# Performance work log

Measured on AMD Instinct MI355X. Metric: run time of the kernel, lower is better.

The kernel has to match this reference:

```python
import jax, jax.numpy as jnp
import numpy as np

B, S, H, E, V, EXTRA = 256, 400, 512, 512, 50257, 100
EMB = H + E  # embedding_size


def setup_inputs() -> dict:
    key = jax.random.key(0)
    ks = jax.random.split(key, 20)
    sd = lambda *shape: 1.0 / np.sqrt(shape[-1])
    d = {
        "input_step": jax.random.normal(ks[0], (B, EMB), jnp.float32),
        "last_hidden": jax.random.normal(ks[1], (1, B, H), jnp.float32),
        "encoder_outputs": jax.random.normal(ks[2], (S, B, H), jnp.float32),
        "enc_batch_extend_vocab": jax.random.randint(ks[3], (S, B), 0, V + EXTRA, jnp.int32),
        "extra_zeros": jnp.zeros((B, EXTRA), jnp.float32),
        "attn_masks": jnp.ones((B, S), jnp.float32),
        "W_ih": jax.random.normal(ks[4], (3 * H, EMB), jnp.float32) * sd(EMB),
        "W_hh": jax.random.normal(ks[5], (3 * H, H), jnp.float32) * sd(H),
        "b_ih": jax.random.normal(ks[6], (3 * H,), jnp.float32) * 0.02,
        "b_hh": jax.random.normal(ks[7], (3 * H,), jnp.float32) * 0.02,
        "attn_W": jax.random.normal(ks[8], (H, 2 * H), jnp.float32) * sd(2 * H),
        "attn_b": jax.random.normal(ks[9], (H,), jnp.float32) * 0.02,
        "attn_v": jax.random.normal(ks[10], (H,), jnp.float32) * sd(H),
        "concat_W": jax.random.normal(ks[11], (H, 2 * H), jnp.float32) * sd(2 * H),
        "concat_b": jax.random.normal(ks[12], (H,), jnp.float32) * 0.02,
        "out_W": jax.random.normal(ks[13], (V, H), jnp.float32) * sd(H),
        "out_b": jax.random.normal(ks[14], (V,), jnp.float32) * 0.02,
        "pgen_W": jax.random.normal(ks[15], (1, 2 * H + EMB), jnp.float32) * sd(2 * H + EMB),
        "pgen_b": jax.random.normal(ks[16], (1,), jnp.float32) * 0.02,
        "sig_W": jax.random.normal(ks[17], (1, H), jnp.float32) * sd(H),
        "sig_b": jax.random.normal(ks[18], (1,), jnp.float32) * 0.02,
    }
    return d


def reference(input_step, last_hidden, encoder_outputs, enc_batch_extend_vocab,
              extra_zeros, attn_masks, W_ih, W_hh, b_ih, b_hh, attn_W, attn_b,
              attn_v, concat_W, concat_b, out_W, out_b, pgen_W, pgen_b,
              sig_W, sig_b):
    # eval-mode dropout is identity
    embedded = input_step                      # [B, EMB]
    h_prev = last_hidden[0]                    # [B, H] (nlayers = 1)

    # --- single GRU step (PyTorch gate layout: r, z, n) ---
    gi = embedded @ W_ih.T + b_ih              # [B, 3H]
    gh = h_prev @ W_hh.T + b_hh                # [B, 3H]
    i_r, i_z, i_n = jnp.split(gi, 3, axis=1)
    h_r, h_z, h_n = jnp.split(gh, 3, axis=1)
    r = jax.nn.sigmoid(i_r + h_r)
    z = jax.nn.sigmoid(i_z + h_z)
    n = jnp.tanh(i_n + r * h_n)
    rnn_output = (1.0 - z) * n + z * h_prev    # [B, H]
    hidden = rnn_output[None]                  # [1, B, H]

    # --- concat attention: v^T tanh(W [h; enc]) over source positions ---
    h_exp = jnp.broadcast_to(rnn_output[None], encoder_outputs.shape)   # [S, B, H]
    energy = jnp.tanh(
        jnp.concatenate([h_exp, encoder_outputs], axis=-1) @ attn_W.T + attn_b
    )                                          # [S, B, H]
    scores = jnp.einsum('sbh,h->bs', energy, attn_v)                    # [B, S]
    scores = jnp.where(attn_masks > 0, scores, jnp.float32(-1e18))
    attn_w = jax.nn.softmax(scores, axis=1)                             # [B, S]
    context = jnp.einsum('bs,sbh->bh', attn_w, encoder_outputs)         # [B, H]

    # --- pgen gate: sigmoid(gelu(Linear([hidden; context; emb]))) ---
    hidden_inp = h_prev                        # last_hidden flattened, [B, H]
    pgen_in = jnp.concatenate([hidden_inp, context, embedded], axis=1)
    pgen = jax.nn.sigmoid(jax.nn.gelu(pgen_in @ pgen_W.T + pgen_b,
                                      approximate=False))               # [B, 1]

    # --- vocab distribution + copy distribution, fused chain ---
    concat_out = jax.nn.gelu(
        jnp.concatenate([rnn_output, context], axis=1) @ concat_W.T + concat_b,
        approximate=False)                     # [B, H]
    logits = concat_out @ out_W.T + out_b      # [B, V]
    vocab_dist = jax.nn.softmax(logits, axis=1)
    vocab_dist = jnp.concatenate([vocab_dist, extra_zeros], axis=1)     # [B, V+EXTRA]
    vocab_dist = pgen * vocab_dist
    attn_dist = (1.0 - pgen) * attn_w          # [B, S]

    idx = enc_batch_extend_vocab.T             # [B, S]
    rows = jnp.arange(vocab_dist.shape[0])[:, None]
    final = vocab_dist.at[rows, idx].add(attn_dist)                     # scatter_add

    out = jax.nn.log_softmax(jnp.log(final + 1e-5), axis=1)

    attn_weights = attn_w.T                    # [S, B]
    sig_hid = rnn_output @ sig_W.T + sig_b     # [B, 1]
    return out, hidden, attn_weights, sig_hid
```

## Files before the change

### kernel.cpp

```cpp
#include <hip/hip_runtime.h>
#include <hip/hip_bf16.h>
#include <math.h>

#define BB 256
#define SS 400
#define HH 512
#define EMBD 1024
#define VV 50257
#define VE 50357
#define O_HID  12891392
#define O_ATT  13022464
#define O_SIG  13124864

typedef __attribute__((ext_vector_type(8))) short s8v;
typedef __attribute__((ext_vector_type(4))) float f4v;

__device__ __forceinline__ float sigmoidf(float x) { return 1.f / (1.f + expf(-x)); }
__device__ __forceinline__ float geluf(float x) { return 0.5f * x * (1.f + erff(x * 0.70710678118654752f)); }

__device__ __forceinline__ void split2_pack(float x0, float x1, unsigned& hp, unsigned& lp) {
  unsigned u0 = __float_as_uint(x0), u1 = __float_as_uint(x1);
  hp = (u0 >> 16) | (u1 & 0xFFFF0000u);
  float d0 = x0 - __uint_as_float(u0 & 0xFFFF0000u);
  float d1 = x1 - __uint_as_float(u1 & 0xFFFF0000u);
  lp = (__float_as_uint(d0) >> 16) | (__float_as_uint(d1) & 0xFFFF0000u);
}

template<int ACT>
__global__ __launch_bounds__(256) void gemm_nt(const float* __restrict__ A, int lda,
                                               const float* __restrict__ W, int ldw,
                                               const float* __restrict__ bias,
                                               float* __restrict__ C, int ldc,
                                               int N, int K) {
  __shared__ __align__(16) float As[16][68];
  __shared__ __align__(16) float Ws[16][68];
  const int tid = threadIdx.x;
  const int m0 = blockIdx.x * 64, n0 = blockIdx.y * 64;
  const int tx = tid & 15, ty = tid >> 4;
  const int lr = tid >> 2;
  const int lk = (tid & 3) * 4;
  float acc[4][4] = {};
  for (int k0 = 0; k0 < K; k0 += 16) {
    float4 a4, w4;
    a4 = *(const float4*)(A + (size_t)(m0 + lr) * lda + k0 + lk);
    int wrow = n0 + lr;
    if (wrow < N) w4 = *(const float4*)(W + (size_t)wrow * ldw + k0 + lk);
    else          w4 = make_float4(0.f, 0.f, 0.f, 0.f);
    __syncthreads();
    As[lk + 0][lr] = a4.x; As[lk + 1][lr] = a4.y; As[lk + 2][lr] = a4.z; As[lk + 3][lr] = a4.w;
    Ws[lk + 0][lr] = w4.x; Ws[lk + 1][lr] = w4.y; Ws[lk + 2][lr] = w4.z; Ws[lk + 3][lr] = w4.w;
    __syncthreads();
#pragma unroll
    for (int k = 0; k < 16; ++k) {
      float4 av = *(const float4*)&As[k][ty * 4];
      float4 wv = *(const float4*)&Ws[k][tx * 4];
      float am[4] = {av.x, av.y, av.z, av.w};
      float wn[4] = {wv.x, wv.y, wv.z, wv.w};
#pragma unroll
      for (int i = 0; i < 4; ++i)
#pragma unroll
        for (int j = 0; j < 4; ++j) acc[i][j] += am[i] * wn[j];
    }
  }
#pragma unroll
  for (int i = 0; i < 4; ++i) {
    int row = m0 + ty * 4 + i;
#pragma unroll
    for (int j = 0; j < 4; ++j) {
      int col = n0 + tx * 4 + j;
      if (col < N) {
        float val = acc[i][j] + bias[col];
        if (ACT == 1) val = geluf(val);
        C[(size_t)row * ldc + col] = val;
      }
    }
  }
}

__global__ __launch_bounds__(256) void gru_gemms(const float* __restrict__ input_step,
                                                 const float* __restrict__ last_hidden,
                                                 const float* __restrict__ W_ih,
                                                 const float* __restrict__ W_hh,
                                                 const float* __restrict__ b_ih,
                                                 const float* __restrict__ b_hh,
                                                 float* __restrict__ gi, float* __restrict__ gh) {
  __shared__ __align__(16) float As[16][68];
  __shared__ __align__(16) float Ws[16][68];
  const bool isGi = blockIdx.y < 24;
  const float* A = isGi ? input_step : last_hidden;
  const float* W = isGi ? W_ih : W_hh;
  const float* bias = isGi ? b_ih : b_hh;
  float* C = isGi ? gi : gh;
  const int lda = isGi ? 1024 : 512;
  const int K = isGi ? 1024 : 512;
  const int n0 = (isGi ? blockIdx.y : blockIdx.y - 24) * 64;
  const int m0 = blockIdx.x * 64;
  const int tid = threadIdx.x;
  const int tx = tid & 15, ty = tid >> 4;
  const int lr = tid >> 2;
  const int lk = (tid & 3) * 4;
  float acc[4][4] = {};
  for (int k0 = 0; k0 < K; k0 += 16) {
    float4 a4 = *(const float4*)(A + (size_t)(m0 + lr) * lda + k0 + lk);
    float4 w4 = *(const float4*)(W + (size_t)(n0 + lr) * lda + k0 + lk);
    __syncthreads();
    As[lk + 0][lr] = a4.x; As[lk + 1][lr] = a4.y; As[lk + 2][lr] = a4.z; As[lk + 3][lr] = a4.w;
    Ws[lk + 0][lr] = w4.x; Ws[lk + 1][lr] = w4.y; Ws[lk + 2][lr] = w4.z; Ws[lk + 3][lr] = w4.w;
    __syncthreads();
#pragma unroll
    for (int k = 0; k < 16; ++k) {
      float4 av = *(const float4*)&As[k][ty * 4];
      float4 wv = *(const float4*)&Ws[k][tx * 4];
      float am[4] = {av.x, av.y, av.z, av.w};
      float wn[4] = {wv.x, wv.y, wv.z, wv.w};
#pragma unroll
      for (int i = 0; i < 4; ++i)
#pragma unroll
        for (int j = 0; j < 4; ++j) acc[i][j] += am[i] * wn[j];
    }
  }
#pragma unroll
  for (int i = 0; i < 4; ++i) {
    int row = m0 + ty * 4 + i;
#pragma unroll
    for (int j = 0; j < 4; ++j) {
      int col = n0 + tx * 4 + j;
      C[(size_t)row * 1536 + col] = acc[i][j] + bias[col];
    }
  }
}

__global__ __launch_bounds__(256) void gru_combine(const float* __restrict__ gi, const float* __restrict__ gh,
                                                   const float* __restrict__ hprev,
                                                   float* __restrict__ rnn, float* __restrict__ hid_out,
                                                   float* __restrict__ cin) {
  int idx = blockIdx.x * 256 + threadIdx.x;
  int b = idx >> 9, j = idx & 511;
  const float* gib = gi + (size_t)b * 1536;
  const float* ghb = gh + (size_t)b * 1536;
  float r = sigmoidf(gib[j] + ghb[j]);
  float z = sigmoidf(gib[512 + j] + ghb[512 + j]);
  float n = tanhf(gib[1024 + j] + r * ghb[1024 + j]);
  float h = hprev[idx];
  float o = (1.f - z) * n + z * h;
  rnn[idx] = o;
  hid_out[idx] = o;
  cin[(size_t)b * 1024 + j] = o;
}

__global__ __launch_bounds__(256) void pack_split(const float* __restrict__ src, int ld, int col0, int rows,
                                                  unsigned short* __restrict__ dhi,
                                                  unsigned short* __restrict__ dlo) {
  int idx = blockIdx.x * 256 + threadIdx.x;
  int l = idx & 63;
  int kb = (idx >> 6) & 15;
  int jb = idx >> 10;
  int j = jb * 16 + (l & 15);
  int k0 = kb * 32 + (l >> 4) * 8;
  float4 x0 = make_float4(0.f, 0.f, 0.f, 0.f), x1 = x0;
  if (j < rows) {
    const float* p = src + (size_t)j * ld + col0 + k0;
    x0 = *(const float4*)p;
    x1 = *(const float4*)(p + 4);
  }
  unsigned h0, l0, h1, l1, h2, l2, h3, l3;
  split2_pack(x0.x, x0.y, h0, l0);
  split2_pack(x0.z, x0.w, h1, l1);
  split2_pack(x1.x, x1.y, h2, l2);
  split2_pack(x1.z, x1.w, h3, l3);
  *(uint4*)(dhi + (size_t)idx * 8) = make_uint4(h0, h1, h2, h3);
  *(uint4*)(dlo + (size_t)idx * 8) = make_uint4(l0, l1, l2, l3);
}

__global__ __launch_bounds__(256, 2) void attn_mfma(const float* __restrict__ enc,
                                                    const unsigned short* __restrict__ BhiP,
                                                    const unsigned short* __restrict__ BloP,
                                                    const float* __restrict__ hW,
                                                    const float* __restrict__ v,
                                                    float* __restrict__ scores) {
  __shared__ __align__(16) unsigned short AhiL[2 * 4 * 66 * 8];
  __shared__ __align__(16) unsigned short AloL[2 * 4 * 66 * 8];

  const int tid = threadIdx.x;
  const int R0 = blockIdx.x * 64;
  const int jhalf = blockIdx.y;
  const int lane = tid & 63;
  const int w = tid >> 6;
  const int jbBase = jhalf * 16 + w * 4;
  const int g = lane >> 4;
  const int l16 = lane & 15;

  const int ar = tid >> 2;
  const int akc = tid & 3;
  const float* aptr = enc + (size_t)(R0 + ar) * 512 + akc * 8;

  const unsigned short* bh0 = BhiP + lane * 8;
  const unsigned short* bl0 = BloP + lane * 8;

  f4v acc[4][4];
#pragma unroll
  for (int rt = 0; rt < 4; ++rt)
#pragma unroll
    for (int ct = 0; ct < 4; ++ct) acc[rt][ct] = (f4v){0.f, 0.f, 0.f, 0.f};

  {
    float4 x0 = *(const float4*)(aptr);
    float4 x1 = *(const float4*)(aptr + 4);
    unsigned h0, l0, h1, l1, h2, l2, h3, l3;
    split2_pack(x0.x, x0.y, h0, l0);
    split2_pack(x0.z, x0.w, h1, l1);
    split2_pack(x1.x, x1.y, h2, l2);
    split2_pack(x1.z, x1.w, h3, l3);
    int wb = akc * 66 + ar;
    *(uint4*)&AhiL[wb * 8] = make_uint4(h0, h1, h2, h3);
    *(uint4*)&AloL[wb * 8] = make_uint4(l0, l1, l2, l3);
  }
  s8v BH[4], BL[4];
#pragma unroll
  for (int ct = 0; ct < 4; ++ct) {
    const int fo = ((jbBase + ct) * 16 + 0) * 512;
    BH[ct] = *(const s8v*)(bh0 + fo);
    BL[ct] = *(const s8v*)(bl0 + fo);
  }
  __syncthreads();

  for (int t = 0; t < 16; ++t) {
    const int k0 = t * 32;
    float4 pa0, pa1;
    if (t < 15) {
      pa0 = *(const float4*)(aptr + k0 + 32);
      pa1 = *(const float4*)(aptr + k0 + 36);
    }
    const int rb = ((t & 1) * 4 + g) * 66 + l16;
#pragma unroll
    for (int rt = 0; rt < 4; ++rt) {
      s8v ah = *(const s8v*)&AhiL[(rb + rt * 16) * 8];
      s8v al = *(const s8v*)&AloL[(rb + rt * 16) * 8];
#pragma unroll
      for (int ct = 0; ct < 4; ++ct) {
        acc[rt][ct] = __builtin_amdgcn_mfma_f32_16x16x32_bf16(ah, BH[ct], acc[rt][ct], 0, 0, 0);
        acc[rt][ct] = __builtin_amdgcn_mfma_f32_16x16x32_bf16(ah, BL[ct], acc[rt][ct], 0, 0, 0);
        acc[rt][ct] = __builtin_amdgcn_mfma_f32_16x16x32_bf16(al, BH[ct], acc[rt][ct], 0, 0, 0);
      }
    }
    if (t < 15) {
#pragma unroll
      for (int ct = 0; ct < 4; ++ct) {
        const int fo = ((jbBase + ct) * 16 + (t + 1)) * 512;
        BH[ct] = *(const s8v*)(bh0 + fo);
        BL[ct] = *(const s8v*)(bl0 + fo);
      }
    }
    if (t < 15) {
      unsigned h0, l0, h1, l1, h2, l2, h3, l3;
      split2_pack(pa0.x, pa0.y, h0, l0);
      split2_pack(pa0.z, pa0.w, h1, l1);
      split2_pack(pa1.x, pa1.y, h2, l2);
      split2_pack(pa1.z, pa1.w, h3, l3);
      int wb = (((t + 1) & 1) * 4 + akc) * 66 + ar;
      *(uint4*)&AhiL[wb * 8] = make_uint4(h0, h1, h2, h3);
      *(uint4*)&AloL[wb * 8] = make_uint4(l0, l1, l2, l3);
    }
    __syncthreads();
  }

  float sp[4][4] = {};
#pragma unroll
  for (int ct = 0; ct < 4; ++ct) {
    int j = jhalf * 256 + w * 64 + ct * 16 + l16;
    float vj = v[j];
    const float* hWj = hW + j;
#pragma unroll
    for (int rt = 0; rt < 4; ++rt) {
#pragma unroll
      for (int q = 0; q < 4; ++q) {
        int rl = rt * 16 + g * 4 + q;
        int b = (R0 + rl) & 255;
        float e = acc[rt][ct][q] + hWj[(size_t)b * 512];
        sp[rt][q] += tanhf(e) * vj;
      }
    }
  }

  __syncthreads();
  float* sredf = (float*)AhiL;
#pragma unroll
  for (int rt = 0; rt < 4; ++rt)
#pragma unroll
    for (int q = 0; q < 4; ++q) {
      float s = sp[rt][q];
      s += __shfl_xor(s, 1); s += __shfl_xor(s, 2);
      s += __shfl_xor(s, 4); s += __shfl_xor(s, 8);
      if (l16 == 0) sredf[(rt * 16 + g * 4 + q) * 4 + w] = s;
    }
  __syncthreads();
  if (tid < 64) {
    float s = sredf[tid * 4 + 0] + sredf[tid * 4 + 1] + sredf[tid * 4 + 2] + sredf[tid * 4 + 3];
    int r = R0 + tid;
    int b = r & 255, si = r >> 8;
    atomicAdd(scores + b * 400 + si, s);
  }
}

__global__ __launch_bounds__(256, 2) void logits_mfma(const float* __restrict__ A,
                                                      const float* __restrict__ W,
                                                      const float* __restrict__ bias,
                                                      float* __restrict__ out) {
  __shared__ __align__(16) unsigned short AhiL[2 * 4 * 66 * 8];
  __shared__ __align__(16) unsigned short AloL[2 * 4 * 66 * 8];

  const int tid = threadIdx.x;
  const int R0 = blockIdx.x * 64;
  const int C0 = blockIdx.y * 256;
  const int lane = tid & 63;
  const int w = tid >> 6;
  const int g = lane >> 4;
  const int l16 = lane & 15;

  const int ar = tid >> 2;
  const int akc = tid & 3;
  const float* aptr = A + (size_t)(R0 + ar) * 512 + akc * 8;

  int jc[4]; bool jok[4];
#pragma unroll
  for (int ct = 0; ct < 4; ++ct) {
    jc[ct] = C0 + w * 64 + ct * 16 + l16;
    jok[ct] = jc[ct] < VV;
  }

  f4v acc[4][4];
#pragma unroll
  for (int rt = 0; rt < 4; ++rt)
#pragma unroll
    for (int ct = 0; ct < 4; ++ct) acc[rt][ct] = (f4v){0.f, 0.f, 0.f, 0.f};

  {
    float4 pa0 = *(const float4*)(aptr);
    float4 pa1 = *(const float4*)(aptr + 4);
    unsigned h0, l0, h1, l1, h2, l2, h3, l3;
    split2_pack(pa0.x, pa0.y, h0, l0);
    split2_pack(pa0.z, pa0.w, h1, l1);
    split2_pack(pa1.x, pa1.y, h2, l2);
    split2_pack(pa1.z, pa1.w, h3, l3);
    int wb = akc * 66 + ar;
    *(uint4*)&AhiL[wb * 8] = make_uint4(h0, h1, h2, h3);
    *(uint4*)&AloL[wb * 8] = make_uint4(l0, l1, l2, l3);
  }
  __syncthreads();

#pragma unroll 2
  for (int t = 0; t < 16; ++t) {
    const int k0 = t * 32;
    s8v BH[4], BL[4];
#pragma unroll
    for (int ct = 0; ct < 4; ++ct) {
      const float* wp = W + (size_t)(jok[ct] ? jc[ct] : 0) * 512 + k0 + g * 8;
      float4 b0 = *(const float4*)wp;
      float4 b1 = *(const float4*)(wp + 4);
      if (!jok[ct]) { b0 = make_float4(0.f, 0.f, 0.f, 0.f); b1 = b0; }
      unsigned h0, l0, h1, l1, h2, l2, h3, l3;
      split2_pack(b0.x, b0.y, h0, l0);
      split2_pack(b0.z, b0.w, h1, l1);
      split2_pack(b1.x, b1.y, h2, l2);
      split2_pack(b1.z, b1.w, h3, l3);
      uint4 ph = make_uint4(h0, h1, h2, h3);
      uint4 pl = make_uint4(l0, l1, l2, l3);
      BH[ct] = *(s8v*)&ph; BL[ct] = *(s8v*)&pl;
    }
    float4 pa0, pa1;
    if (t < 15) {
      pa0 = *(const float4*)(aptr + k0 + 32);
      pa1 = *(const float4*)(aptr + k0 + 36);
    }
    const int rb = ((t & 1) * 4 + g) * 66 + l16;
#pragma unroll
    for (int rt = 0; rt < 4; ++rt) {
      s8v ah = *(const s8v*)&AhiL[(rb + rt * 16) * 8];
      s8v al = *(const s8v*)&AloL[(rb + rt * 16) * 8];
#pragma unroll
      for (int ct = 0; ct < 4; ++ct) {
        acc[rt][ct] = __builtin_amdgcn_mfma_f32_16x16x32_bf16(ah, BH[ct], acc[rt][ct], 0, 0, 0);
        acc[rt][ct] = __builtin_amdgcn_mfma_f32_16x16x32_bf16(ah, BL[ct], acc[rt][ct], 0, 0, 0);
        acc[rt][ct] = __builtin_amdgcn_mfma_f32_16x16x32_bf16(al, BH[ct], acc[rt][ct], 0, 0, 0);
      }
    }
    if (t < 15) {
      unsigned h0, l0, h1, l1, h2, l2, h3, l3;
      split2_pack(pa0.x, pa0.y, h0, l0);
      split2_pack(pa0.z, pa0.w, h1, l1);
      split2_pack(pa1.x, pa1.y, h2, l2);
      split2_pack(pa1.z, pa1.w, h3, l3);
      int wb = (((t + 1) & 1) * 4 + akc) * 66 + ar;
      *(uint4*)&AhiL[wb * 8] = make_uint4(h0, h1, h2, h3);
      *(uint4*)&AloL[wb * 8] = make_uint4(l0, l1, l2, l3);
    }
    __syncthreads();
  }

#pragma unroll
  for (int ct = 0; ct < 4; ++ct) {
    if (!jok[ct]) continue;
    float bj = bias[jc[ct]];
#pragma unroll
    for (int rt = 0; rt < 4; ++rt) {
      int row = R0 + rt * 16 + g * 4;
#pragma unroll
      for (int q = 0; q < 4; ++q)
        out[(size_t)(row + q) * VE + jc[ct]] = acc[rt][ct][q] + bj;
    }
  }
}

__global__ __launch_bounds__(256) void softmax_k(const float* __restrict__ scores,
                                                 const float* __restrict__ masks,
                                                 float* __restrict__ attnw, float* __restrict__ attnT) {
  int b = blockIdx.x, tid = threadIdx.x;
  __shared__ float red[4];
  float m = -3e38f;
  for (int s = tid; s < 400; s += 256) {
    float sc = (masks[b * 400 + s] > 0.f) ? scores[b * 400 + s] : -1e18f;
    m = fmaxf(m, sc);
  }
#pragma unroll
  for (int o = 32; o; o >>= 1) m = fmaxf(m, __shfl_xor(m, o));
  if ((tid & 63) == 0) red[tid >> 6] = m;
  __syncthreads();
  m = fmaxf(fmaxf(red[0], red[1]), fmaxf(red[2], red[3]));
  __syncthreads();
  float z = 0.f;
  for (int s = tid; s < 400; s += 256) {
    float sc = (masks[b * 400 + s] > 0.f) ? scores[b * 400 + s] : -1e18f;
    z += expf(sc - m);
  }
#pragma unroll
  for (int o = 32; o; o >>= 1) z += __shfl_xor(z, o);
  if ((tid & 63) == 0) red[tid >> 6] = z;
  __syncthreads();
  z = red[0] + red[1] + red[2] + red[3];
  float inv = 1.f / z;
  for (int s = tid; s < 400; s += 256) {
    float sc = (masks[b * 400 + s] > 0.f) ? scores[b * 400 + s] : -1e18f;
    float w = expf(sc - m) * inv;
    attnw[b * 400 + s] = w;
    attnT[s * 256 + b] = w;
  }
}

__global__ __launch_bounds__(1024) void context_k(const float* __restrict__ enc,
                                                  const float* __restrict__ attnw,
                                                  float* __restrict__ ctx, float* __restrict__ cin) {
  int b = blockIdx.x, tid = threadIdx.x;
  __shared__ float w[400];
  __shared__ float part[4][512];
  for (int s = tid; s < 400; s += 1024) w[s] = attnw[b * 400 + s];
  __syncthreads();
  const int h = (tid & 255) * 2;
  const int sq = tid >> 8;
  const float* p = enc + (size_t)b * 512 + h;
  float cx = 0.f, cy = 0.f;
  const int s0 = sq * 100;
#pragma unroll 4
  for (int s = s0; s < s0 + 100; ++s) {
    float2 e = *(const float2*)(p + (size_t)s * 131072);
    cx += w[s] * e.x; cy += w[s] * e.y;
  }
  part[sq][h] = cx; part[sq][h + 1] = cy;
  __syncthreads();
  if (tid < 512) {
    float vsum = part[0][tid] + part[1][tid] + part[2][tid] + part[3][tid];
    ctx[(size_t)b * 512 + tid] = vsum;
    cin[(size_t)b * 1024 + 512 + tid] = vsum;
  }
}

__global__ __launch_bounds__(256) void pgen_k(const float* __restrict__ hprev, const float* __restrict__ ctx,
                                              const float* __restrict__ emb, const float* __restrict__ pW,
                                              const float* __restrict__ pb, float* __restrict__ pgen) {
  int b = blockIdx.x, tid = threadIdx.x;
  float acc = 0.f;
  for (int k = tid; k < 2048; k += 256) {
    float x = (k < 512) ? hprev[(size_t)b * 512 + k]
            : (k < 1024) ? ctx[(size_t)b * 512 + k - 512]
            : emb[(size_t)b * 1024 + k - 1024];
    acc += x * pW[k];
  }
#pragma unroll
  for (int o = 32; o; o >>= 1) acc += __shfl_xor(acc, o);
  __shared__ float red[4];
  if ((tid & 63) == 0) red[tid >> 6] = acc;
  __syncthreads();
  if (tid == 0) {
    float d = red[0] + red[1] + red[2] + red[3] + pb[0];
    pgen[b] = sigmoidf(geluf(d));
  }
}

__global__ void sig_k(const float* __restrict__ rnn, const float* __restrict__ sW,
                      const float* __restrict__ sb, float* __restrict__ outp) {
  int b = blockIdx.x, tid = threadIdx.x;
  float acc = 0.f;
  for (int k = tid; k < 512; k += 64) acc += rnn[(size_t)b * 512 + k] * sW[k];
#pragma unroll
  for (int o = 32; o; o >>= 1) acc += __shfl_xor(acc, o);
  if (tid == 0) outp[b] = acc + sb[0];
}

__global__ __launch_bounds__(1024) void rowscale_k(float* __restrict__ out, const float* __restrict__ pgen) {
  const int b = blockIdx.x, tid = threadIdx.x;
  float* row = out + (size_t)b * VE;
  __shared__ float red[16];
  float m = -3e38f;
  for (int j = tid * 4; j < 50256; j += 4096) {
    float4 x = *(const float4*)(row + j);
    m = fmaxf(fmaxf(m, fmaxf(x.x, x.y)), fmaxf(x.z, x.w));
  }
  if (tid == 0) m = fmaxf(m, row[50256]);
#pragma unroll
  for (int o = 32; o; o >>= 1) m = fmaxf(m, __shfl_xor(m, o));
  if ((tid & 63) == 0) red[tid >> 6] = m;
  __syncthreads();
  m = red[0];
#pragma unroll
  for (int i = 1; i < 16; ++i) m = fmaxf(m, red[i]);
  __syncthreads();
  float z = 0.f;
  for (int j = tid * 4; j < 50256; j += 4096) {
    float4 x = *(const float4*)(row + j);
    z += expf(x.x - m) + expf(x.y - m) + expf(x.z - m) + expf(x.w - m);
  }
  if (tid == 0) z += expf(row[50256] - m);
#pragma unroll
  for (int o = 32; o; o >>= 1) z += __shfl_xor(z, o);
  if ((tid & 63) == 0) red[tid >> 6] = z;
  __syncthreads();
  z = 0.f;
#pragma unroll
  for (int i = 0; i < 16; ++i) z += red[i];
  const float coef = pgen[b] / z;
  for (int j = tid * 4; j < 50356; j += 4096) {
    float4 x = *(const float4*)(row + j);
    float4 y;
    y.x = (j + 0 < VV) ? coef * expf(x.x - m) : 0.f;
    y.y = (j + 1 < VV) ? coef * expf(x.y - m) : 0.f;
    y.z = (j + 2 < VV) ? coef * expf(x.z - m) : 0.f;
    y.w = (j + 3 < VV) ? coef * expf(x.w - m) : 0.f;
    *(float4*)(row + j) = y;
  }
  if (tid == 0) row[50356] = 0.f;
}

__global__ __launch_bounds__(256) void scatter_k(float* __restrict__ out, const int* __restrict__ ebev,
                                                 const float* __restrict__ attnw, const float* __restrict__ pgen) {
  int t = blockIdx.x * 256 + threadIdx.x;
  int s = t >> 8, b = t & 255;
  int idx = ebev[t];
  float w = (1.f - pgen[b]) * attnw[b * 400 + s];
  atomicAdd(out + (size_t)b * VE + idx, w);
}

__global__ __launch_bounds__(1024) void sumfinal_k(float* __restrict__ out) {
  const int b = blockIdx.x, tid = threadIdx.x;
  float* row = out + (size_t)b * VE;
  __shared__ float red[16];
  float t = 0.f;
  for (int j = tid * 4; j < 50356; j += 4096) {
    float4 x = *(const float4*)(row + j);
    t += x.x + x.y + x.z + x.w;
  }
  if (tid == 0) t += row[50356];
#pragma unroll
  for (int o = 32; o; o >>= 1) t += __shfl_xor(t, o);
  if ((tid & 63) == 0) red[tid >> 6] = t;
  __syncthreads();
  float tot = 0.f;
#pragma unroll
  for (int i = 0; i < 16; ++i) tot += red[i];
  const float logT = logf(tot + (float)VE * 1e-5f);
  for (int j = tid * 4; j < 50356; j += 4096) {
    float4 x = *(const float4*)(row + j);
    x.x = logf(x.x + 1e-5f) - logT;
    x.y = logf(x.y + 1e-5f) - logT;
    x.z = logf(x.z + 1e-5f) - logT;
    x.w = logf(x.w + 1e-5f) - logT;
    *(float4*)(row + j) = x;
  }
  if (tid == 0) row[50356] = logf(row[50356] + 1e-5f) - logT;
}

extern "C" void kernel_launch(void* const* d_in, const int* in_sizes, int n_in,
                              void* d_out, int out_size, void* d_ws, size_t ws_size,
                              hipStream_t stream) {
  const float* input_step = (const float*)d_in[0];
  const float* last_hidden = (const float*)d_in[1];
  const float* enc = (const float*)d_in[2];
  const int*   ebev = (const int*)d_in[3];
  const float* masks = (const float*)d_in[5];
  const float* W_ih = (const float*)d_in[6];
  const float* W_hh = (const float*)d_in[7];
  const float* b_ih = (const float*)d_in[8];
  const float* b_hh = (const float*)d_in[9];
  const float* attn_W = (const float*)d_in[10];
  const float* attn_b = (const float*)d_in[11];
  const float* attn_v = (const float*)d_in[12];
  const float* concat_W = (const float*)d_in[13];
  const float* concat_b = (const float*)d_in[14];
  const float* out_W = (const float*)d_in[15];
  const float* out_b = (const float*)d_in[16];
  const float* pgen_W = (const float*)d_in[17];
  const float* pgen_b = (const float*)d_in[18];
  const float* sig_W = (const float*)d_in[19];
  const float* sig_b = (const float*)d_in[20];

  float* out = (float*)d_out;
  float* ws = (float*)d_ws;
  float* gi     = ws;
  float* gh     = gi + 393216;
  float* rnn    = gh + 393216;
  float* hW     = rnn + 131072;
  float* scores = hW + 131072;
  float* attnw  = scores + 102400;
  float* ctx    = attnw + 102400;
  float* cin    = ctx + 131072;
  float* cout_  = cin + 262144;
  float* pgen   = cout_ + 131072;
  float* rowm   = pgen + 256;
  float* coef   = rowm + 256;
  float* logT   = coef + 256;
  unsigned short* Bhi = (unsigned short*)(logT + 256);
  unsigned short* Blo = Bhi + 262144;

  pack_split<<<128, 256, 0, stream>>>(attn_W, 1024, 512, 512, Bhi, Blo);
  hipMemsetAsync(scores, 0, 102400 * sizeof(float), stream);
  gru_gemms<<<dim3(4, 48), 256, 0, stream>>>(input_step, last_hidden, W_ih, W_hh, b_ih, b_hh, gi, gh);
  gru_combine<<<512, 256, 0, stream>>>(gi, gh, last_hidden, rnn, out + O_HID, cin);
  gemm_nt<0><<<dim3(4, 8), 256, 0, stream>>>(rnn, 512, attn_W, 1024, attn_b, hW, 512, 512, 512);
  attn_mfma<<<dim3(1600, 2), 256, 0, stream>>>(enc, Bhi, Blo, hW, attn_v, scores);
  softmax_k<<<256, 256, 0, stream>>>(scores, masks, attnw, out + O_ATT);
  context_k<<<256, 1024, 0, stream>>>(enc, attnw, ctx, cin);
  pgen_k<<<256, 256, 0, stream>>>(last_hidden, ctx, input_step, pgen_W, pgen_b, pgen);
  sig_k<<<256, 64, 0, stream>>>(rnn, sig_W, sig_b, out + O_SIG);
  gemm_nt<1><<<dim3(4, 8), 256, 0, stream>>>(cin, 1024, concat_W, 1024, concat_b, cout_, 512, 512, 1024);
  logits_mfma<<<dim3(4, 197), 256, 0, stream>>>(cout_, out_W, out_b, out);
  rowscale_k<<<256, 1024, 0, stream>>>(out, pgen);
  scatter_k<<<400, 256, 0, stream>>>(out, ebev, attnw, pgen);
  sumfinal_k<<<256, 1024, 0, stream>>>(out);
}
```

Baseline: 587.7 us.

## Merge attention column halves into one 512-thread block, drop atomics and memset

The attention-score MFMA kernel now covers all 512 hidden columns in a single 512-thread block (8 waves) instead of two blocks over column halves. Each encoder tile is loaded and split into bf16 hi/lo pairs once instead of twice. Because one block now owns each full row sum, scores are written directly rather than atomically added, and the scores memset is removed. The larger block holds one block per CU under the launch bounds, which may reduce latency hiding and change register pressure.

```diff
diff --git a/kernel.cpp b/kernel.cpp
--- a/kernel.cpp
+++ b/kernel.cpp
@@ -172,7 +172,7 @@
   *(uint4*)(dlo + (size_t)idx * 8) = make_uint4(l0, l1, l2, l3);
 }
 
-__global__ __launch_bounds__(256, 2) void attn_mfma(const float* __restrict__ enc,
+__global__ __launch_bounds__(512, 1) void attn_mfma(const float* __restrict__ enc,
                                                     const unsigned short* __restrict__ BhiP,
                                                     const unsigned short* __restrict__ BloP,
                                                     const float* __restrict__ hW,
@@ -183,16 +183,17 @@
 
   const int tid = threadIdx.x;
   const int R0 = blockIdx.x * 64;
-  const int jhalf = blockIdx.y;
   const int lane = tid & 63;
   const int w = tid >> 6;
-  const int jbBase = jhalf * 16 + w * 4;
+  const int jbBase = w * 4;
   const int g = lane >> 4;
   const int l16 = lane & 15;
 
-  const int ar = tid >> 2;
-  const int akc = tid & 3;
-  const float* aptr = enc + (size_t)(R0 + ar) * 512 + akc * 8;
+  const int ar = tid >> 3;
+  const int ac8 = tid & 7;
+  const int akc = ac8 >> 1;
+  const int ahalf = ac8 & 1;
+  const float* aptr = enc + (size_t)(R0 + ar) * 512 + ac8 * 4;
 
   const unsigned short* bh0 = BhiP + lane * 8;
   const unsigned short* bl0 = BloP + lane * 8;
@@ -205,15 +206,12 @@
 
   {
     float4 x0 = *(const float4*)(aptr);
-    float4 x1 = *(const float4*)(aptr + 4);
-    unsigned h0, l0, h1, l1, h2, l2, h3, l3;
+    unsigned h0, l0, h1, l1;
     split2_pack(x0.x, x0.y, h0, l0);
     split2_pack(x0.z, x0.w, h1, l1);
-    split2_pack(x1.x, x1.y, h2, l2);
-    split2_pack(x1.z, x1.w, h3, l3);
-    int wb = akc * 66 + ar;
-    *(uint4*)&AhiL[wb * 8] = make_uint4(h0, h1, h2, h3);
-    *(uint4*)&AloL[wb * 8] = make_uint4(l0, l1, l2, l3);
+    int wb = (akc * 66 + ar) * 8 + ahalf * 4;
+    *(uint2*)&AhiL[wb] = make_uint2(h0, h1);
+    *(uint2*)&AloL[wb] = make_uint2(l0, l1);
   }
   s8v BH[4], BL[4];
 #pragma unroll
@@ -226,10 +224,9 @@
 
   for (int t = 0; t < 16; ++t) {
     const int k0 = t * 32;
-    float4 pa0, pa1;
+    float4 pa0;
     if (t < 15) {
       pa0 = *(const float4*)(aptr + k0 + 32);
-      pa1 = *(const float4*)(aptr + k0 + 36);
     }
     const int rb = ((t & 1) * 4 + g) * 66 + l16;
 #pragma unroll
@@ -252,14 +249,12 @@
       }
     }
     if (t < 15) {
-      unsigned h0, l0, h1, l1, h2, l2, h3, l3;
+      unsigned h0, l0, h1, l1;
       split2_pack(pa0.x, pa0.y, h0, l0);
       split2_pack(pa0.z, pa0.w, h1, l1);
-      split2_pack(pa1.x, pa1.y, h2, l2);
-      split2_pack(pa1.z, pa1.w, h3, l3);
-      int wb = (((t + 1) & 1) * 4 + akc) * 66 + ar;
-      *(uint4*)&AhiL[wb * 8] = make_uint4(h0, h1, h2, h3);
-      *(uint4*)&AloL[wb * 8] = make_uint4(l0, l1, l2, l3);
+      int wb = ((((t + 1) & 1) * 4 + akc) * 66 + ar) * 8 + ahalf * 4;
+      *(uint2*)&AhiL[wb] = make_uint2(h0, h1);
+      *(uint2*)&AloL[wb] = make_uint2(l0, l1);
     }
     __syncthreads();
   }
@@ -267,7 +262,7 @@
   float sp[4][4] = {};
 #pragma unroll
   for (int ct = 0; ct < 4; ++ct) {
-    int j = jhalf * 256 + w * 64 + ct * 16 + l16;
+    int j = w * 64 + ct * 16 + l16;
     float vj = v[j];
     const float* hWj = hW + j;
 #pragma unroll
@@ -291,14 +286,16 @@
       float s = sp[rt][q];
       s += __shfl_xor(s, 1); s += __shfl_xor(s, 2);
       s += __shfl_xor(s, 4); s += __shfl_xor(s, 8);
-      if (l16 == 0) sredf[(rt * 16 + g * 4 + q) * 4 + w] = s;
+      if (l16 == 0) sredf[(rt * 16 + g * 4 + q) * 8 + w] = s;
     }
   __syncthreads();
   if (tid < 64) {
-    float s = sredf[tid * 4 + 0] + sredf[tid * 4 + 1] + sredf[tid * 4 + 2] + sredf[tid * 4 + 3];
+    float s = 0.f;
+#pragma unroll
+    for (int i = 0; i < 8; ++i) s += sredf[tid * 8 + i];
     int r = R0 + tid;
     int b = r & 255, si = r >> 8;
-    atomicAdd(scores + b * 400 + si, s);
+    scores[b * 400 + si] = s;
   }
 }
 
@@ -630,11 +627,10 @@
   unsigned short* Blo = Bhi + 262144;
 
   pack_split<<<128, 256, 0, stream>>>(attn_W, 1024, 512, 512, Bhi, Blo);
-  hipMemsetAsync(scores, 0, 102400 * sizeof(float), stream);
   gru_gemms<<<dim3(4, 48), 256, 0, stream>>>(input_step, last_hidden, W_ih, W_hh, b_ih, b_hh, gi, gh);
   gru_combine<<<512, 256, 0, stream>>>(gi, gh, last_hidden, rnn, out + O_HID, cin);
   gemm_nt<0><<<dim3(4, 8), 256, 0, stream>>>(rnn, 512, attn_W, 1024, attn_b, hW, 512, 512, 512);
-  attn_mfma<<<dim3(1600, 2), 256, 0, stream>>>(enc, Bhi, Blo, hW, attn_v, scores);
+  attn_mfma<<<1600, 512, 0, stream>>>(enc, Bhi, Blo, hW, attn_v, scores);
   softmax_k<<<256, 256, 0, stream>>>(scores, masks, attnw, out + O_ATT);
   context_k<<<256, 1024, 0, stream>>>(enc, attnw, ctx, cin);
   pgen_k<<<256, 256, 0, stream>>>(last_hidden, ctx, input_step, pgen_W, pgen_b, pgen);
```

Result: slower. 641.9 us (+9.2%).
